# Performance work log

Hardware: AMD Instinct MI355X
Metric: run time of the kernel (lower is better)

Reference implementation:

```python
import jax, jax.numpy as jnp
import numpy as np

B, S, IN = 1024, 256, 8
H = 512
F = 96  # forecast_len
OUT = 1


def _lstm_step(h, c, x, Wih, Whh, bih, bhh):
    # PyTorch gate order: i, f, g, o
    gates = x @ Wih.T + h @ Whh.T + (bih + bhh)  # [B, 4H]
    i, f, g, o = jnp.split(gates, 4, axis=-1)
    i = jax.nn.sigmoid(i)
    f = jax.nn.sigmoid(f)
    g = jnp.tanh(g)
    o = jax.nn.sigmoid(o)
    c_new = f * c + i * g
    h_new = o * jnp.tanh(c_new)
    return h_new, c_new


def setup_inputs() -> dict:
    key = jax.random.key(0)
    ks = jax.random.split(key, 12)
    s_in = 1.0 / np.sqrt(H)
    def u(k, shape):
        return jax.random.uniform(k, shape, jnp.float32, -s_in, s_in)
    return {
        "x": jax.random.normal(ks[0], (B, S, IN), jnp.float32),
        "enc_Wih": u(ks[1], (4 * H, IN)),
        "enc_Whh": u(ks[2], (4 * H, H)),
        "enc_bih": u(ks[3], (4 * H,)),
        "enc_bhh": u(ks[4], (4 * H,)),
        "dec_Wih": u(ks[5], (4 * H, OUT)),
        "dec_Whh": u(ks[6], (4 * H, H)),
        "dec_bih": u(ks[7], (4 * H,)),
        "dec_bhh": u(ks[8], (4 * H,)),
        "out_W": u(ks[9], (OUT, H)),
        "out_b": u(ks[10], (OUT,)),
    }


def reference(x, enc_Wih, enc_Whh, enc_bih, enc_bhh,
              dec_Wih, dec_Whh, dec_bih, dec_bhh, out_W, out_b):
    batch = x.shape[0]
    h0 = jnp.zeros((batch, H), x.dtype)
    c0 = jnp.zeros((batch, H), x.dtype)

    # ---- Encoder: scan over time ----
    def enc_step(carry, xt):
        h, c = carry
        h, c = _lstm_step(h, c, xt, enc_Wih, enc_Whh, enc_bih, enc_bhh)
        return (h, c), None

    xs = jnp.swapaxes(x, 0, 1)  # [S, B, IN]
    (h, c), _ = jax.lax.scan(enc_step, (h0, c0), xs)

    y0 = jnp.zeros((batch, OUT), x.dtype)

    def dec_step(carry, _):
        h, c, y = carry
        h, c = _lstm_step(h, c, y, dec_Wih, dec_Whh, dec_bih, dec_bhh)
        pred = h @ out_W.T + out_b  # [B, 1]
        return (h, c, pred), pred

    _, preds = jax.lax.scan(dec_step, (h, c, y0), None, length=F)  # [F, B, 1]
    return jnp.swapaxes(preds[..., 0], 0, 1)  # [B, F]
```

## Files before the change

### kernel.cpp

```cpp
#include <hip/hip_runtime.h>


#define Hh 512
#define K2 544
#define BATCH 1024
#define SEQ 256
#define FCAST 96
#define Mrows 64
#define SAS 552
#define SHS 40

typedef _Float16 f16;
typedef _Float16 f16x8 __attribute__((ext_vector_type(8)));
typedef float f32x4 __attribute__((ext_vector_type(4)));

__device__ __forceinline__ float sigf(float v) { return 1.0f / (1.0f + __expf(-v)); }
__device__ __forceinline__ float tanhf_(float v) { return 1.0f - 2.0f / (__expf(2.0f * v) + 1.0f); }

__device__ __forceinline__ f16x8 ld16(const f16* p, bool byp) {
  f16x8 d;
  if (byp) asm volatile("global_load_dwordx4 %0, %1, off sc0 sc1" : "=v"(d) : "v"(p) : "memory");
  else     asm volatile("global_load_dwordx4 %0, %1, off sc0"     : "=v"(d) : "v"(p) : "memory");
  return d;
}
__device__ __forceinline__ void st16(f16* p, f16x8 v, bool byp) {
  if (byp) asm volatile("global_store_dwordx4 %0, %1, off sc0 sc1" :: "v"(p), "v"(v) : "memory");
  else     asm volatile("global_store_dwordx4 %0, %1, off"         :: "v"(p), "v"(v) : "memory");
}
__device__ __forceinline__ int atomic_add_l2(int* p, int v) {
  int old;
  asm volatile("global_atomic_add %0, %1, %2, off sc0\n\ts_waitcnt vmcnt(0)"
               : "=v"(old) : "v"(p), "v"(v) : "memory");
  return old;
}

__global__ void prep_weights(const float* __restrict__ encWih, const float* __restrict__ encWhh,
                             const float* __restrict__ decWih, const float* __restrict__ decWhh,
                             const float* __restrict__ encBih, const float* __restrict__ encBhh,
                             const float* __restrict__ decBih, const float* __restrict__ decBhh,
                             const float* __restrict__ outW, const float* __restrict__ outB,
                             f16* __restrict__ encT, f16* __restrict__ decPW, f16* __restrict__ decFW,
                             float* __restrict__ bE, float* __restrict__ bP, float* __restrict__ bF) {
  int id = blockIdx.x * 256 + threadIdx.x;
  if (id >= 2048 * 68) return;
  int n = id / 68, c8 = id % 68;
  int nslot = n >> 7, c = n & 127, w = c >> 5, cc = c & 31, ct = cc >> 4, l4v = cc & 15;
  int g = ct * 2 + (l4v >> 3), j = l4v & 7;
  int unit = nslot * 32 + w * 8 + j, r = g * Hh + unit;
  size_t o = (size_t)n * K2 + c8 * 8;
  if (c8 < 64) {
    float dwih = decWih[r];
#pragma unroll
    for (int e = 0; e < 8; ++e) {
      int k = c8 * 8 + e;
      encT[o + e] = (f16)encWhh[(size_t)r * Hh + k];
      float dw = decWhh[(size_t)r * Hh + k];
      decPW[o + e] = (f16)dw;
      decFW[o + e] = (f16)(dw + outW[k] * dwih);
    }
  } else if (c8 == 64) {
#pragma unroll
    for (int e = 0; e < 8; ++e) {
      encT[o + e] = (f16)encWih[r * 8 + e];
      decPW[o + e] = (f16)0.f;
      decFW[o + e] = (f16)0.f;
    }
  } else {
#pragma unroll
    for (int e = 0; e < 8; ++e) {
      encT[o + e] = (f16)0.f;
      decPW[o + e] = (f16)0.f;
      decFW[o + e] = (f16)0.f;
    }
  }
  if (c8 == 0) {
    bE[n] = encBih[r] + encBhh[r];
    float bd = decBih[r] + decBhh[r];
    bP[n] = bd;
    bF[n] = bd + outB[0] * decWih[r];
  }
}

__global__ void init_state(f16* __restrict__ h0, float* __restrict__ out,
                           const float* __restrict__ outB, int* __restrict__ sync) {
  int i = blockIdx.x * 256 + threadIdx.x;
  if (i < BATCH * Hh) h0[i] = (f16)0.f;
  if (i < BATCH * FCAST) out[i] = outB[0];
  if (i < 2048) sync[i] = 0;
}

__global__ __launch_bounds__(256, 1) void lstm_persist(
    const f16* __restrict__ encT, const f16* __restrict__ decPW, const f16* __restrict__ decFW,
    const float* __restrict__ bE, const float* __restrict__ bP, const float* __restrict__ bF,
    const float* __restrict__ x, f16* __restrict__ h0, f16* __restrict__ h1,
    float* __restrict__ out, const float* __restrict__ outW, int* __restrict__ sync) {
  __shared__ __align__(16) f16 sA[Mrows * SAS];
  __shared__ __align__(16) f16 sH[Mrows * SHS];
  __shared__ int sInfo[2];

  int* cnt = sync;
  int* slots = sync + 1024;
  int* arrive = sync + 1032;

  const int T = threadIdx.x;
  const int w = T >> 6, lane = T & 63, l4 = lane & 15, q = lane >> 4;
  const int j = l4 & 7;
  const bool lo = (l4 < 8);

  int xcd;
  asm("s_getreg_b32 %0, hwreg(HW_REG_XCC_ID)" : "=s"(xcd));
  xcd &= 7;

  if (T == 0) {
    int r = __hip_atomic_fetch_add(&slots[xcd], 1, __ATOMIC_RELAXED, __HIP_MEMORY_SCOPE_AGENT);
    sInfo[0] = r;
    __hip_atomic_fetch_add(arrive, 1, __ATOMIC_RELAXED, __HIP_MEMORY_SCOPE_AGENT);
    while (__hip_atomic_load(arrive, __ATOMIC_RELAXED, __HIP_MEMORY_SCOPE_AGENT) < 256)
      __builtin_amdgcn_s_sleep(2);
    int ok = 1;
    for (int xx = 0; xx < 8; ++xx)
      ok &= (__hip_atomic_load(&slots[xx], __ATOMIC_RELAXED, __HIP_MEMORY_SCOPE_AGENT) == 32);
    sInfo[1] = ok;
  }
  __syncthreads();
  const int rank = sInfo[0];
  const bool uni = (sInfo[1] != 0);
  int group, nslot;
  if (uni) { group = xcd * 2 + (rank >> 4); nslot = rank & 15; }
  else     { group = (int)blockIdx.x >> 4;  nslot = (int)blockIdx.x & 15; }
  const int m0 = group * Mrows, n0 = nslot * 128, u0 = nslot * 32;
  int* myCnt = cnt + group * 32;

  f16x8 bw[2][17];
  float bias_r[4];
  float cst[2][4];
#pragma unroll
  for (int a = 0; a < 2; ++a)
#pragma unroll
    for (int r = 0; r < 4; ++r) cst[a][r] = 0.f;

  const int myUnit = u0 + w * 8 + j;

  auto loadB = [&](const f16* WT, const float* bias) {
#pragma unroll
    for (int ct = 0; ct < 2; ++ct) {
      const f16* base = &WT[(size_t)(n0 + w * 32 + ct * 16 + l4) * K2 + q * 8];
#pragma unroll
      for (int ks = 0; ks < 17; ++ks) bw[ct][ks] = *(const f16x8*)(base + ks * 32);
    }
#pragma unroll
    for (int g = 0; g < 4; ++g)
      bias_r[g] = bias[n0 + w * 32 + (g >> 1) * 16 + (g & 1) * 8 + j];
  };

  loadB(encT, bE);
  float ow_r = 0.f;

  for (int s = 0; s < SEQ + FCAST; ++s) {
    const bool enc = s < SEQ;
    if (s == SEQ) {
      loadB(decPW, bP);
      ow_r = outW[myUnit];
    } else if (s == SEQ + 1) {
      loadB(decFW, bF);
    }

    if (s > 0) {
      asm volatile("s_waitcnt vmcnt(0)" ::: "memory");
      __syncthreads();
      if (T == 0) {
        if (uni) {
          atomic_add_l2(myCnt, 1);
          while (atomic_add_l2(myCnt, 0) < 16 * s) __builtin_amdgcn_s_sleep(1);
        } else {
          __hip_atomic_fetch_add(myCnt, 1, __ATOMIC_RELAXED, __HIP_MEMORY_SCOPE_AGENT);
          while (__hip_atomic_load(myCnt, __ATOMIC_RELAXED, __HIP_MEMORY_SCOPE_AGENT) < 16 * s)
            __builtin_amdgcn_s_sleep(2);
        }
      }
      __syncthreads();
    }

    const f16* hin = (s & 1) ? h1 : h0;
    f16* hout = (s & 1) ? h0 : h1;

#pragma unroll
    for (int b = 0; b < 2; ++b) {
      f16x8 d[8];
#pragma unroll
      for (int jj = 0; jj < 8; ++jj) {
        int id = T + 256 * (b * 8 + jj);
        int row = id >> 6, c8 = (id & 63) * 8;
        d[jj] = ld16(&hin[(size_t)(m0 + row) * Hh + c8], !uni);
      }
      asm volatile("s_waitcnt vmcnt(0)" ::: "memory");
#pragma unroll
      for (int jj = 0; jj < 8; ++jj) {
        int id = T + 256 * (b * 8 + jj);
        int row = id >> 6, c8 = (id & 63) * 8;
        *(f16x8*)&sA[row * SAS + c8] = d[jj];
      }
    }
    if (enc && T < Mrows) {
      const float* xp = &x[((size_t)(m0 + T) * SEQ + s) * 8];
      float4 xa = *(const float4*)xp, xb = *(const float4*)(xp + 4);
      f16x8 xv = {(f16)xa.x, (f16)xa.y, (f16)xa.z, (f16)xa.w,
                  (f16)xb.x, (f16)xb.y, (f16)xb.z, (f16)xb.w};
      f16x8 z = {(f16)0.f, (f16)0.f, (f16)0.f, (f16)0.f, (f16)0.f, (f16)0.f, (f16)0.f, (f16)0.f};
      *(f16x8*)&sA[T * SAS + 512] = xv;
      *(f16x8*)&sA[T * SAS + 520] = z;
      *(f16x8*)&sA[T * SAS + 528] = z;
      *(f16x8*)&sA[T * SAS + 536] = z;
    }
    __syncthreads();

    f32x4 acc[4][2];
#pragma unroll
    for (int a = 0; a < 4; ++a)
#pragma unroll
      for (int c = 0; c < 2; ++c) acc[a][c] = (f32x4){0.f, 0.f, 0.f, 0.f};

    auto innerK = [&](int ks) {
      int ko = ks * 32 + q * 8;
#pragma unroll
      for (int at = 0; at < 4; ++at) {
        f16x8 af = *(const f16x8*)&sA[(at * 16 + l4) * SAS + ko];
        acc[at][0] = __builtin_amdgcn_mfma_f32_16x16x32_f16(af, bw[0][ks], acc[at][0], 0, 0, 0);
        acc[at][1] = __builtin_amdgcn_mfma_f32_16x16x32_f16(af, bw[1][ks], acc[at][1], 0, 0, 0);
      }
    };
    if (enc) {
#pragma unroll
      for (int ks = 0; ks < 17; ++ks) innerK(ks);
    } else {
#pragma unroll
      for (int ks = 0; ks < 16; ++ks) innerK(ks);
    }

#pragma unroll
    for (int ah = 0; ah < 2; ++ah) {
#pragma unroll
      for (int r = 0; r < 4; ++r) {
        int atL = ah;
        int atH = ah + 2;
        float xiL = acc[atL][0][r], xgL = acc[atL][1][r];
        float xiH = acc[atH][0][r], xgH = acc[atH][1][r];
        float pf_recv = __shfl_xor(lo ? xiL : xiH, 8, 16);
        float po_recv = 0.f;
        {
          float payload0 = lo ? xiH : xiL;
          float payload1 = lo ? xgH : xgL;
          pf_recv = __shfl_xor(payload0, 8, 16);
          po_recv = __shfl_xor(payload1, 8, 16);
        }
        float gi = lo ? xiL : pf_recv;
        float gf = lo ? pf_recv : xiH;
        float gg_ = lo ? xgL : po_recv;
        float go = lo ? po_recv : xgH;
        float pi = gi + bias_r[0];
        float pf = gf + bias_r[1];
        float pg = gg_ + bias_r[2];
        float po = go + bias_r[3];
        float ig = sigf(pi), fg = sigf(pf), gg = tanhf_(pg), og = sigf(po);
        float cn = fg * cst[ah][r] + ig * gg;
        cst[ah][r] = cn;
        float hn = og * tanhf_(cn);
        int at = lo ? atL : atH;
        int row = at * 16 + q * 4 + r;
        sH[row * SHS + w * 8 + j] = (f16)hn;
        if (!enc) {
          float pp = hn * ow_r;
          pp += __shfl_xor(pp, 1, 16);
          pp += __shfl_xor(pp, 2, 16);
          pp += __shfl_xor(pp, 4, 16);
          if (j == 0) atomicAdd(&out[(m0 + row) * FCAST + (s - SEQ)], pp);
        }
      }
    }
    __syncthreads();

    {
      int row = T >> 2, seg = T & 3;
      f16x8 hv = *(const f16x8*)&sH[row * SHS + seg * 8];
      st16(&hout[(size_t)(m0 + row) * Hh + u0 + seg * 8], hv, !uni);
    }
  }
}

extern "C" void kernel_launch(void* const* d_in, const int* in_sizes, int n_in, void* d_out,
                              int out_size, void* d_ws, size_t ws_size, hipStream_t stream) {
  const float* x = (const float*)d_in[0];
  const float* encWih = (const float*)d_in[1];
  const float* encWhh = (const float*)d_in[2];
  const float* encBih = (const float*)d_in[3];
  const float* encBhh = (const float*)d_in[4];
  const float* decWih = (const float*)d_in[5];
  const float* decWhh = (const float*)d_in[6];
  const float* decBih = (const float*)d_in[7];
  const float* decBhh = (const float*)d_in[8];
  const float* outW = (const float*)d_in[9];
  const float* outB = (const float*)d_in[10];
  float* out = (float*)d_out;

  char* ws = (char*)d_ws;
  f16* encT = (f16*)ws;
  f16* decPW = encT + 2048 * K2;
  f16* decFW = decPW + 2048 * K2;
  f16* h0 = decFW + 2048 * K2;
  f16* h1 = h0 + BATCH * Hh;
  float* bE = (float*)(h1 + BATCH * Hh);
  float* bP = bE + 2048;
  float* bF = bP + 2048;
  int* sync = (int*)(bF + 2048);

  prep_weights<<<544, 256, 0, stream>>>(encWih, encWhh, decWih, decWhh, encBih, encBhh, decBih,
                                        decBhh, outW, outB, encT, decPW, decFW, bE, bP, bF);
  init_state<<<2048, 256, 0, stream>>>(h0, out, outB, sync);
  lstm_persist<<<256, 256, 0, stream>>>(encT, decPW, decFW, bE, bP, bF, x, h0, h1, out, outW, sync);
}
```

Measured before the change: 2.613 ms.

## Split each block's row tile across two wave groups with 512 threads

```diff
diff --git a/kernel.cpp b/kernel.cpp
--- a/kernel.cpp
+++ b/kernel.cpp
@@ -89,7 +89,7 @@
   if (i < 2048) sync[i] = 0;
 }
 
-__global__ __launch_bounds__(256, 1) void lstm_persist(
+__global__ __launch_bounds__(512, 2) void lstm_persist(
     const f16* __restrict__ encT, const f16* __restrict__ decPW, const f16* __restrict__ decFW,
     const float* __restrict__ bE, const float* __restrict__ bP, const float* __restrict__ bF,
     const float* __restrict__ x, f16* __restrict__ h0, f16* __restrict__ h1,
@@ -103,7 +103,9 @@
   int* arrive = sync + 1032;
 
   const int T = threadIdx.x;
-  const int w = T >> 6, lane = T & 63, l4 = lane & 15, q = lane >> 4;
+  const int wv = T >> 6, lane = T & 63, l4 = lane & 15, q = lane >> 4;
+  const int w = wv & 3;
+  const int mh = wv >> 2;
   const int j = l4 & 7;
   const bool lo = (l4 < 8);
 
@@ -133,11 +135,9 @@
 
   f16x8 bw[2][17];
   float bias_r[4];
-  float cst[2][4];
-#pragma unroll
-  for (int a = 0; a < 2; ++a)
-#pragma unroll
-    for (int r = 0; r < 4; ++r) cst[a][r] = 0.f;
+  float cst[4];
+#pragma unroll
+  for (int r = 0; r < 4; ++r) cst[r] = 0.f;
 
   const int myUnit = u0 + w * 8 + j;
 
@@ -184,19 +184,18 @@
     const f16* hin = (s & 1) ? h1 : h0;
     f16* hout = (s & 1) ? h0 : h1;
 
-#pragma unroll
-    for (int b = 0; b < 2; ++b) {
+    {
       f16x8 d[8];
 #pragma unroll
       for (int jj = 0; jj < 8; ++jj) {
-        int id = T + 256 * (b * 8 + jj);
+        int id = T + 512 * jj;
         int row = id >> 6, c8 = (id & 63) * 8;
         d[jj] = ld16(&hin[(size_t)(m0 + row) * Hh + c8], !uni);
       }
       asm volatile("s_waitcnt vmcnt(0)" ::: "memory");
 #pragma unroll
       for (int jj = 0; jj < 8; ++jj) {
-        int id = T + 256 * (b * 8 + jj);
+        int id = T + 512 * jj;
         int row = id >> 6, c8 = (id & 63) * 8;
         *(f16x8*)&sA[row * SAS + c8] = d[jj];
       }
@@ -214,17 +213,17 @@
     }
     __syncthreads();
 
-    f32x4 acc[4][2];
-#pragma unroll
-    for (int a = 0; a < 4; ++a)
+    f32x4 acc[2][2];
+#pragma unroll
+    for (int a = 0; a < 2; ++a)
 #pragma unroll
       for (int c = 0; c < 2; ++c) acc[a][c] = (f32x4){0.f, 0.f, 0.f, 0.f};
 
     auto innerK = [&](int ks) {
       int ko = ks * 32 + q * 8;
 #pragma unroll
-      for (int at = 0; at < 4; ++at) {
-        f16x8 af = *(const f16x8*)&sA[(at * 16 + l4) * SAS + ko];
+      for (int at = 0; at < 2; ++at) {
+        f16x8 af = *(const f16x8*)&sA[(mh * 32 + at * 16 + l4) * SAS + ko];
         acc[at][0] = __builtin_amdgcn_mfma_f32_16x16x32_f16(af, bw[0][ks], acc[at][0], 0, 0, 0);
         acc[at][1] = __builtin_amdgcn_mfma_f32_16x16x32_f16(af, bw[1][ks], acc[at][1], 0, 0, 0);
       }
@@ -238,48 +237,39 @@
     }
 
 #pragma unroll
-    for (int ah = 0; ah < 2; ++ah) {
-#pragma unroll
-      for (int r = 0; r < 4; ++r) {
-        int atL = ah;
-        int atH = ah + 2;
-        float xiL = acc[atL][0][r], xgL = acc[atL][1][r];
-        float xiH = acc[atH][0][r], xgH = acc[atH][1][r];
-        float pf_recv = __shfl_xor(lo ? xiL : xiH, 8, 16);
-        float po_recv = 0.f;
-        {
-          float payload0 = lo ? xiH : xiL;
-          float payload1 = lo ? xgH : xgL;
-          pf_recv = __shfl_xor(payload0, 8, 16);
-          po_recv = __shfl_xor(payload1, 8, 16);
-        }
-        float gi = lo ? xiL : pf_recv;
-        float gf = lo ? pf_recv : xiH;
-        float gg_ = lo ? xgL : po_recv;
-        float go = lo ? po_recv : xgH;
-        float pi = gi + bias_r[0];
-        float pf = gf + bias_r[1];
-        float pg = gg_ + bias_r[2];
-        float po = go + bias_r[3];
-        float ig = sigf(pi), fg = sigf(pf), gg = tanhf_(pg), og = sigf(po);
-        float cn = fg * cst[ah][r] + ig * gg;
-        cst[ah][r] = cn;
-        float hn = og * tanhf_(cn);
-        int at = lo ? atL : atH;
-        int row = at * 16 + q * 4 + r;
-        sH[row * SHS + w * 8 + j] = (f16)hn;
-        if (!enc) {
-          float pp = hn * ow_r;
-          pp += __shfl_xor(pp, 1, 16);
-          pp += __shfl_xor(pp, 2, 16);
-          pp += __shfl_xor(pp, 4, 16);
-          if (j == 0) atomicAdd(&out[(m0 + row) * FCAST + (s - SEQ)], pp);
-        }
+    for (int r = 0; r < 4; ++r) {
+      float xiL = acc[0][0][r], xgL = acc[0][1][r];
+      float xiH = acc[1][0][r], xgH = acc[1][1][r];
+      float payload0 = lo ? xiH : xiL;
+      float payload1 = lo ? xgH : xgL;
+      float pf_recv = __shfl_xor(payload0, 8, 16);
+      float po_recv = __shfl_xor(payload1, 8, 16);
+      float gi = lo ? xiL : pf_recv;
+      float gf = lo ? pf_recv : xiH;
+      float gg_ = lo ? xgL : po_recv;
+      float go = lo ? po_recv : xgH;
+      float pi = gi + bias_r[0];
+      float pf = gf + bias_r[1];
+      float pg = gg_ + bias_r[2];
+      float po = go + bias_r[3];
+      float ig = sigf(pi), fg = sigf(pf), gg = tanhf_(pg), og = sigf(po);
+      float cn = fg * cst[r] + ig * gg;
+      cst[r] = cn;
+      float hn = og * tanhf_(cn);
+      int at = lo ? 0 : 1;
+      int row = mh * 32 + at * 16 + q * 4 + r;
+      sH[row * SHS + w * 8 + j] = (f16)hn;
+      if (!enc) {
+        float pp = hn * ow_r;
+        pp += __shfl_xor(pp, 1, 16);
+        pp += __shfl_xor(pp, 2, 16);
+        pp += __shfl_xor(pp, 4, 16);
+        if (j == 0) atomicAdd(&out[(m0 + row) * FCAST + (s - SEQ)], pp);
       }
     }
     __syncthreads();
 
-    {
+    if (T < 256) {
       int row = T >> 2, seg = T & 3;
       f16x8 hv = *(const f16x8*)&sH[row * SHS + seg * 8];
       st16(&hout[(size_t)(m0 + row) * Hh + u0 + seg * 8], hv, !uni);
@@ -316,5 +306,5 @@
   prep_weights<<<544, 256, 0, stream>>>(encWih, encWhh, decWih, decWhh, encBih, encBhh, decBih,
                                         decBhh, outW, outB, encT, decPW, decFW, bE, bP, bF);
   init_state<<<2048, 256, 0, stream>>>(h0, out, outB, sync);
-  lstm_persist<<<256, 256, 0, stream>>>(encT, decPW, decFW, bE, bP, bF, x, h0, h1, out, outW, sync);
-}
+  lstm_persist<<<256, 512, 0, stream>>>(encT, decPW, decFW, bE, bP, bF, x, h0, h1, out, outW, sync);
+}
```

Result: slower. 4.804 ms (+83.8%).

## Overlap second half of h-state load with MFMA on first half rows

Applied to the files above, without the earlier changes.

```diff
diff --git a/kernel.cpp b/kernel.cpp
--- a/kernel.cpp
+++ b/kernel.cpp
@@ -184,26 +184,55 @@
     const f16* hin = (s & 1) ? h1 : h0;
     f16* hout = (s & 1) ? h0 : h1;
 
-#pragma unroll
-    for (int b = 0; b < 2; ++b) {
-      f16x8 d[8];
-#pragma unroll
-      for (int jj = 0; jj < 8; ++jj) {
-        int id = T + 256 * (b * 8 + jj);
-        int row = id >> 6, c8 = (id & 63) * 8;
-        d[jj] = ld16(&hin[(size_t)(m0 + row) * Hh + c8], !uni);
-      }
-      asm volatile("s_waitcnt vmcnt(0)" ::: "memory");
-#pragma unroll
-      for (int jj = 0; jj < 8; ++jj) {
-        int id = T + 256 * (b * 8 + jj);
-        int row = id >> 6, c8 = (id & 63) * 8;
-        *(f16x8*)&sA[row * SAS + c8] = d[jj];
-      }
-    }
-    if (enc && T < Mrows) {
+    f16x8 d[16];
+#pragma unroll
+    for (int jj = 0; jj < 16; ++jj) {
+      int id = T + 256 * jj;
+      int row = id >> 6, c8 = (id & 63) * 8;
+      d[jj] = ld16(&hin[(size_t)(m0 + row) * Hh + c8], !uni);
+    }
+    const bool hasx = enc && (T < Mrows);
+    float4 xa, xb;
+    if (hasx) {
       const float* xp = &x[((size_t)(m0 + T) * SEQ + s) * 8];
-      float4 xa = *(const float4*)xp, xb = *(const float4*)(xp + 4);
+      xa = *(const float4*)xp;
+      xb = *(const float4*)(xp + 4);
+    }
+    asm volatile("s_waitcnt vmcnt(8)" ::: "memory");
+#pragma unroll
+    for (int jj = 0; jj < 8; ++jj) {
+      int id = T + 256 * jj;
+      int row = id >> 6, c8 = (id & 63) * 8;
+      *(f16x8*)&sA[row * SAS + c8] = d[jj];
+    }
+    __syncthreads();
+
+    f32x4 acc[4][2];
+#pragma unroll
+    for (int a = 0; a < 4; ++a)
+#pragma unroll
+      for (int c = 0; c < 2; ++c) acc[a][c] = (f32x4){0.f, 0.f, 0.f, 0.f};
+
+    auto mac = [&](int at, int ks) {
+      int ko = ks * 32 + q * 8;
+      f16x8 af = *(const f16x8*)&sA[(at * 16 + l4) * SAS + ko];
+      acc[at][0] = __builtin_amdgcn_mfma_f32_16x16x32_f16(af, bw[0][ks], acc[at][0], 0, 0, 0);
+      acc[at][1] = __builtin_amdgcn_mfma_f32_16x16x32_f16(af, bw[1][ks], acc[at][1], 0, 0, 0);
+    };
+#pragma unroll
+    for (int ks = 0; ks < 16; ++ks) {
+      mac(0, ks);
+      mac(1, ks);
+    }
+
+    asm volatile("s_waitcnt vmcnt(0)" ::: "memory");
+#pragma unroll
+    for (int jj = 8; jj < 16; ++jj) {
+      int id = T + 256 * jj;
+      int row = id >> 6, c8 = (id & 63) * 8;
+      *(f16x8*)&sA[row * SAS + c8] = d[jj];
+    }
+    if (hasx) {
       f16x8 xv = {(f16)xa.x, (f16)xa.y, (f16)xa.z, (f16)xa.w,
                   (f16)xb.x, (f16)xb.y, (f16)xb.z, (f16)xb.w};
       f16x8 z = {(f16)0.f, (f16)0.f, (f16)0.f, (f16)0.f, (f16)0.f, (f16)0.f, (f16)0.f, (f16)0.f};
@@ -214,27 +243,18 @@
     }
     __syncthreads();
 
-    f32x4 acc[4][2];
-#pragma unroll
-    for (int a = 0; a < 4; ++a)
-#pragma unroll
-      for (int c = 0; c < 2; ++c) acc[a][c] = (f32x4){0.f, 0.f, 0.f, 0.f};
-
-    auto innerK = [&](int ks) {
-      int ko = ks * 32 + q * 8;
-#pragma unroll
-      for (int at = 0; at < 4; ++at) {
-        f16x8 af = *(const f16x8*)&sA[(at * 16 + l4) * SAS + ko];
-        acc[at][0] = __builtin_amdgcn_mfma_f32_16x16x32_f16(af, bw[0][ks], acc[at][0], 0, 0, 0);
-        acc[at][1] = __builtin_amdgcn_mfma_f32_16x16x32_f16(af, bw[1][ks], acc[at][1], 0, 0, 0);
-      }
-    };
     if (enc) {
-#pragma unroll
-      for (int ks = 0; ks < 17; ++ks) innerK(ks);
-    } else {
-#pragma unroll
-      for (int ks = 0; ks < 16; ++ks) innerK(ks);
+      mac(0, 16);
+      mac(1, 16);
+    }
+#pragma unroll
+    for (int ks = 0; ks < 16; ++ks) {
+      mac(2, ks);
+      mac(3, ks);
+    }
+    if (enc) {
+      mac(2, 16);
+      mac(3, 16);
     }
 
 #pragma unroll
@@ -245,14 +265,10 @@
         int atH = ah + 2;
         float xiL = acc[atL][0][r], xgL = acc[atL][1][r];
         float xiH = acc[atH][0][r], xgH = acc[atH][1][r];
-        float pf_recv = __shfl_xor(lo ? xiL : xiH, 8, 16);
-        float po_recv = 0.f;
-        {
-          float payload0 = lo ? xiH : xiL;
-          float payload1 = lo ? xgH : xgL;
-          pf_recv = __shfl_xor(payload0, 8, 16);
-          po_recv = __shfl_xor(payload1, 8, 16);
-        }
+        float payload0 = lo ? xiH : xiL;
+        float payload1 = lo ? xgH : xgL;
+        float pf_recv = __shfl_xor(payload0, 8, 16);
+        float po_recv = __shfl_xor(payload1, 8, 16);
         float gi = lo ? xiL : pf_recv;
         float gf = lo ? pf_recv : xiH;
         float gg_ = lo ? xgL : po_recv;
```

Measured after the change: 2.451 ms. -6.2%, faster.
